# Performance work log

Measured on AMD Instinct MI355X. Metric: run time of the kernel, lower is better.

## Reference

```python
import jax, jax.numpy as jnp
import numpy as np

N = 50000        # nodes
E = 800000       # directed edges
NUM_E = 10000    # hyperedges
NFEAT, NHID, NOUT = 256, 128, 64
K = 10
TEMP = 5.0


def gcn_prop(h, src, dst, n):
    # PyG GCNConv propagation with added self-loops: D^-1/2 (A+I) D^-1/2 h
    ew = jnp.ones(src.shape[0], h.dtype)
    deg = 1.0 + jax.ops.segment_sum(ew, dst, num_segments=n)  # self-loop adds 1
    dinv = jax.lax.rsqrt(deg)
    norm = dinv[src] * dinv[dst]                   # [E]
    out = jax.ops.segment_sum(h[src] * norm[:, None], dst, num_segments=n)
    out = out + h / deg[:, None]                   # self-loop term (weight deg^-1)
    return out


def gcn_conv(x, W, b, src, dst, n):
    return gcn_prop(x @ W, src, dst, n) + b


def hgnnp_conv(x, W, b, hv, he, n, num_e):
    # dhg HGNNPConv: theta(x) then v->e mean aggregation, then e->v mean
    h = x @ W + b
    ones = jnp.ones(hv.shape[0], h.dtype)
    e_deg = jnp.maximum(jax.ops.segment_sum(ones, he, num_segments=num_e), 1.0)
    v_deg = jnp.maximum(jax.ops.segment_sum(ones, hv, num_segments=n), 1.0)
    e_feat = jax.ops.segment_sum(h[hv], he, num_segments=num_e) / e_deg[:, None]
    v_out = jax.ops.segment_sum(e_feat[he], hv, num_segments=n) / v_deg[:, None]
    return v_out


def setup_inputs() -> dict:
    key = jax.random.key(0)
    ks = jax.random.split(key, 12)
    x = jax.random.normal(ks[0], (N, NFEAT), jnp.float32)
    edge_index = jax.random.randint(ks[1], (2, E), 0, N)
    hv_idx = jax.random.randint(ks[2], (200000,), 0, N)
    he_idx = jax.random.randint(ks[3], (200000,), 0, NUM_E)

    def glorot(k, shape):
        lim = float(np.sqrt(6.0 / (shape[0] + shape[1])))
        return jax.random.uniform(k, shape, jnp.float32, -lim, lim)

    return {
        "x": x, "edge_index": edge_index, "hv_idx": hv_idx, "he_idx": he_idx,
        "gcn_W1": glorot(ks[4], (NFEAT, NHID)), "gcn_b1": jnp.zeros((NHID,), jnp.float32),
        "gcn_W2": glorot(ks[5], (NHID, NOUT)), "gcn_b2": jnp.zeros((NOUT,), jnp.float32),
        "hg_W1": glorot(ks[6], (NFEAT, NHID)), "hg_b1": jnp.zeros((NHID,), jnp.float32),
        "hg_W2": glorot(ks[7], (NHID, NOUT)), "hg_b2": jnp.zeros((NOUT,), jnp.float32),
        "num_iter": 1,
    }


def reference(x, edge_index, hv_idx, he_idx,
              gcn_W1, gcn_b1, gcn_W2, gcn_b2,
              hg_W1, hg_b1, hg_W2, hg_b2, num_iter):
    src, dst = edge_index[0], edge_index[1]

    # HGNNP_GCN encoder (dropout is identity in eval-style reference)
    x1 = jax.nn.relu(gcn_conv(x, gcn_W1, gcn_b1, src, dst, N))
    x2 = gcn_conv(x1, gcn_W2, gcn_b2, src, dst, N)
    x3 = jax.nn.relu(hgnnp_conv(x, hg_W1, hg_b1, hv_idx, he_idx, N, NUM_E))
    x4 = hgnnp_conv(x3, hg_W2, hg_b2, hv_idx, he_idx, N, NUM_E)  # is_last: no act
    embeds = x2 * 0.5 + x4 * 0.5                     # [N, NOUT]

    # row-normalize (diag(1/||row||) @ data)
    data = embeds / jnp.linalg.norm(embeds, axis=1, keepdims=True)

    # kmeans++ init is a host-side, data-dependent pick; use deterministic
    # strided row selection from the (detached) normalized embeddings.
    init_idx = jnp.arange(K) * (N // K)
    mu = jax.lax.stop_gradient(data[init_idx])       # [K, NOUT]

    for _ in range(int(num_iter)):
        dist = data @ mu.T                           # [N, K]
        r = jax.nn.softmax(TEMP * dist, axis=1)
        cluster_r = r.sum(axis=0)                    # [K]
        cluster_mean = r.T @ data                    # [K, NOUT]
        mu = cluster_mean / cluster_r[:, None]

    dist = data @ mu.T
    r = jax.nn.softmax(TEMP * dist, axis=1)
    return mu, r, embeds, dist
```

## Files before the change

kernel.cpp:

```cpp
#include <hip/hip_runtime.h>
#include <hip/hip_bf16.h>


#define NN   50000
#define NP   50048
#define EE   800000
#define NINC 200000
#define NEH  10000
#define KCL  10

#define MU_OFF  0
#define R_OFF   640
#define EMB_OFF 500640
#define D_OFF   3700640

typedef __hip_bfloat16 bf16;
typedef unsigned short u16;
typedef unsigned int   u32;
typedef __attribute__((ext_vector_type(8))) short short8;
typedef __attribute__((ext_vector_type(4))) float f32x4;

__device__ __forceinline__ float b2f(bf16 v){ return __bfloat162float(v); }
__device__ __forceinline__ float us2f(u16 u){ return __uint_as_float(((unsigned)u) << 16); }
__device__ __forceinline__ u16 f2bu(float f){
  unsigned u = __float_as_uint(f);
  return (u16)((u + 0x7fffu + ((u >> 16) & 1u)) >> 16);
}
__device__ __forceinline__ bf16 f2b(float f){
  u16 r = f2bu(f);
  bf16 h;
  reinterpret_cast<u16&>(h) = r;
  return h;
}
__device__ __forceinline__ float ldf(const void* p, size_t i, int isbf){
  return isbf ? b2f(((const bf16*)p)[i]) : ((const float*)p)[i];
}
__device__ __forceinline__ void stf(void* p, size_t i, float v, int isbf){
  if (isbf) ((bf16*)p)[i] = f2b(v);
  else      ((float*)p)[i] = v;
}

__global__ void k_detect(const u16* __restrict__ xr, int* flag){
  __shared__ int bad;
  if (threadIdx.x == 0) bad = 0;
  __syncthreads();
  for (int i = threadIdx.x; i < 4096; i += 256){
    int e = (xr[i] >> 7) & 0xFF;
    if (e >= 0xEF) bad = 1;
  }
  __syncthreads();
  if (threadIdx.x == 0) *flag = bad ? 0 : 1;
}

__global__ void k_aconv(const void* __restrict__ x, u16* __restrict__ xb,
                        const int* __restrict__ flag){
  int i = blockIdx.x*256 + threadIdx.x;
  const int n4 = NN*256/4;
  if (i >= n4) return;
  ushort4 o;
  if (flag[0]){
    o = ((const ushort4*)x)[i];
  } else {
    float4 v = ((const float4*)x)[i];
    o = make_ushort4(f2bu(v.x), f2bu(v.y), f2bu(v.z), f2bu(v.w));
  }
  ((ushort4*)xb)[i] = o;
}

__global__ void k_wprep(const void* gW1, const void* hW1, const void* gW2, const void* hW2,
                        const void* gb1, const void* hb1, const void* gb2, const void* hb2,
                        u16* gW1t, u16* hW1t, u16* gW2t, u16* hW2t,
                        float* gb1f, float* hb1f, float* gb2f, float* hb2f,
                        const int* __restrict__ flag){
  const int isbf = flag[0];
  int i = blockIdx.x*256 + threadIdx.x;
  if (i < 256*128){
    int n = i >> 8, k = i & 255;
    gW1t[i] = f2bu(ldf(gW1, (size_t)k*128 + n, isbf));
    hW1t[i] = f2bu(ldf(hW1, (size_t)k*128 + n, isbf));
  }
  if (i < 64*128){
    int n = i >> 7, k = i & 127;
    gW2t[i] = f2bu(ldf(gW2, (size_t)k*64 + n, isbf));
    hW2t[i] = f2bu(ldf(hW2, (size_t)k*64 + n, isbf));
  }
  if (i < 128){ gb1f[i] = ldf(gb1,i,isbf); hb1f[i] = ldf(hb1,i,isbf); }
  if (i < 64) { gb2f[i] = ldf(gb2,i,isbf); hb2f[i] = ldf(hb2,i,isbf); }
}

template<int WORDS, int NRANGE, int NCHUNK>
__global__ __launch_bounds__(256) void k_hist(const int* __restrict__ key,
                                              u32* __restrict__ H, int chunk){
  __shared__ u32 hist[WORDS];
  int r = blockIdx.x / NCHUNK, c = blockIdx.x % NCHUNK;
  for (int i = threadIdx.x; i < WORDS; i += 256) hist[i] = 0;
  __syncthreads();
  int base = c*chunk, lo = r*2*WORDS;
  for (int i = threadIdx.x; i < chunk; i += 256){
    int d = key[base+i] - lo;
    if ((unsigned)d < (unsigned)(2*WORDS))
      atomicAdd(&hist[d < WORDS ? d : d-WORDS], d < WORDS ? 1u : 65536u);
  }
  __syncthreads();
  u32* out = H + (size_t)blockIdx.x*WORDS;
  for (int i = threadIdx.x; i < WORDS; i += 256) out[i] = hist[i];
}

template<int WORDS, int NRANGE, int NCHUNK>
__global__ void k_hscan(u32* __restrict__ H, int* __restrict__ cnt){
  int t = blockIdx.x*256 + threadIdx.x;
  if (t >= NRANGE*WORDS) return;
  int r = t / WORDS, w = t % WORDS;
  u32 run = 0;
  u32* col = H + (size_t)r*NCHUNK*WORDS + w;
  for (int b = 0; b < NCHUNK; ++b){
    u32 v = col[(size_t)b*WORDS];
    col[(size_t)b*WORDS] = run;
    run += v;
  }
  cnt[r*2*WORDS + w]         = (int)(run & 0xffffu);
  cnt[r*2*WORDS + WORDS + w] = (int)(run >> 16);
}

template<int WORDS, int NRANGE, int NCHUNK>
__global__ __launch_bounds__(256) void k_fill2(const int* __restrict__ key,
    const int* __restrict__ val, const u32* __restrict__ H,
    const int* __restrict__ rp, int* __restrict__ csr, int chunk){
  __shared__ u32 cur[WORDS];
  int r = blockIdx.x / NCHUNK, c = blockIdx.x % NCHUNK;
  const u32* pre = H + (size_t)blockIdx.x*WORDS;
  for (int i = threadIdx.x; i < WORDS; i += 256) cur[i] = pre[i];
  __syncthreads();
  int base = c*chunk, lo = r*2*WORDS;
  for (int i = threadIdx.x; i < chunk; i += 256){
    int dd = key[base+i];
    int d = dd - lo;
    if ((unsigned)d < (unsigned)(2*WORDS)){
      bool low = d < WORDS;
      u32 old = atomicAdd(&cur[low ? d : d-WORDS], low ? 1u : 65536u);
      u32 rank = low ? (old & 0xffffu) : (old >> 16);
      csr[rp[dd] + (int)rank] = val[base+i];
    }
  }
}

__global__ void k_invs(const int* __restrict__ cg, const int* __restrict__ cv,
                       const int* __restrict__ ce,
                       float* dinv, float* invv, float* inve){
  int i = blockIdx.x*256 + threadIdx.x;
  if (i < NN){
    float d = 1.0f + (float)cg[i];
    dinv[i] = rsqrtf(d);
    invv[i] = 1.0f / fmaxf((float)cv[i], 1.0f);
  } else if (i < NP){
    dinv[i] = 0.f;
  }
  if (i < NEH) inve[i] = 1.0f / fmaxf((float)ce[i], 1.0f);
}

__global__ void k_scan1_all(const int* cg, const int* cv, const int* ce,
                            int* rp_g, int* rp_v, int* rp_e,
                            int* bs_g, int* bs_v, int* bs_e){
  const int blk = blockIdx.x;
  const int* in; int* out; int* bsum; int n; int lb;
  if (blk < 196){ in=cg; out=rp_g; bsum=bs_g; n=NN; lb=blk; }
  else if (blk < 392){ in=cv; out=rp_v; bsum=bs_v; n=NN; lb=blk-196; }
  else { in=ce; out=rp_e; bsum=bs_e; n=NEH; lb=blk-392; }
  __shared__ int s[256];
  int t = threadIdx.x, i = lb*256 + t;
  int v = (i < n) ? in[i] : 0;
  s[t] = v; __syncthreads();
  #pragma unroll
  for (int off = 1; off < 256; off <<= 1){
    int add = (t >= off) ? s[t-off] : 0;
    __syncthreads();
    s[t] += add;
    __syncthreads();
  }
  if (i < n) out[i] = s[t] - v;
  if (t == 255) bsum[lb] = s[255];
}

__global__ void k_scan2_all(int* bs_g, int* bs_v, int* bs_e){
  int* bsum; int nb;
  if (blockIdx.x == 0){ bsum = bs_g; nb = 196; }
  else if (blockIdx.x == 1){ bsum = bs_v; nb = 196; }
  else { bsum = bs_e; nb = 40; }
  __shared__ int s[256];
  int t = threadIdx.x;
  int v = (t < nb) ? bsum[t] : 0;
  s[t] = v; __syncthreads();
  #pragma unroll
  for (int off = 1; off < 256; off <<= 1){
    int add = (t >= off) ? s[t-off] : 0;
    __syncthreads();
    s[t] += add;
    __syncthreads();
  }
  if (t < nb) bsum[t] = s[t] - v;
}

__global__ void k_scan3_all(int* rp_g, int* rp_v, int* rp_e,
                            const int* bs_g, const int* bs_v, const int* bs_e){
  const int blk = blockIdx.x;
  int* rp; const int* bsum; int n; int lb;
  if (blk < 196){ rp=rp_g; bsum=bs_g; n=NN; lb=blk; }
  else if (blk < 392){ rp=rp_v; bsum=bs_v; n=NN; lb=blk-196; }
  else { rp=rp_e; bsum=bs_e; n=NEH; lb=blk-392; }
  int i = lb*256 + threadIdx.x;
  if (i < n) rp[i] += bsum[lb];
}

template<int KDIM, int NCOL>
__global__ __launch_bounds__(256) void k_gemm_mfma(
    const u16* __restrict__ A, const u16* __restrict__ Wt,
    const float* __restrict__ bias, const float* __restrict__ rowscale,
    u16* __restrict__ C, int relu)
{
  constexpr int NT  = NCOL/16;
  constexpr int LDA = 40;
  __shared__ __align__(16) u16 Asl[64][LDA];
  __shared__ __align__(16) u16 Wsl[NCOL][LDA];
  const int tid  = threadIdx.x;
  const int wave = tid >> 6, lane = tid & 63;
  const int l15 = lane & 15, l4 = lane >> 4;
  const int row0 = blockIdx.x * 64;
  const int ar = tid >> 2, aq = tid & 3;
  constexpr int NW = NCOL*4/256;

  f32x4 acc[NT] = {};

  for (int kk = 0; kk < KDIM; kk += 32){
    {
      uint4 v = *(const uint4*)(A + (size_t)(row0 + ar)*KDIM + kk + aq*8);
      *(uint4*)&Asl[ar][aq*8] = v;
    }
    #pragma unroll
    for (int w2 = 0; w2 < NW; ++w2){
      int c = tid + w2*256;
      int n = c >> 2, q = c & 3;
      uint4 v = *(const uint4*)(Wt + (size_t)n*KDIM + kk + q*8);
      *(uint4*)&Wsl[n][q*8] = v;
    }
    __syncthreads();
    short8 af = *(const short8*)&Asl[wave*16 + l15][l4*8];
    #pragma unroll
    for (int t = 0; t < NT; ++t){
      short8 bf = *(const short8*)&Wsl[t*16 + l15][l4*8];
      acc[t] = __builtin_amdgcn_mfma_f32_16x16x32_bf16(af, bf, acc[t], 0, 0, 0);
    }
    __syncthreads();
  }

  #pragma unroll
  for (int t = 0; t < NT; ++t){
    int gcol = t*16 + l15;
    float b = bias ? bias[gcol] : 0.f;
    #pragma unroll
    for (int e = 0; e < 4; ++e){
      int grow = row0 + wave*16 + l4*4 + e;
      float v = acc[t][e] + b;
      if (relu) v = fmaxf(v, 0.f);
      if (rowscale) v *= rowscale[grow];
      C[(size_t)grow*NCOL + gcol] = f2bu(v);
    }
  }
}

template<int F, bool OUTBF, bool SELF>
__global__ __launch_bounds__(256) void k_gather(
    const int* __restrict__ rp, const int* __restrict__ cnt,
    const int* __restrict__ csr, const float* __restrict__ scale,
    const u16* __restrict__ h, const float* __restrict__ bias,
    void* __restrict__ out, int relu)
{
  const int wave = threadIdx.x >> 6, lane = threadIdx.x & 63;
  const int d = blockIdx.x*4 + wave;
  const int k0 = rp[d], n = cnt[d];

  if constexpr (F == 128){
    const uint* h32 = (const uint*)h;
    float a0=0,a1=0,b0=0,b1=0,c0=0,c1=0,e0=0,e1=0;
    if (SELF){
      uint v = h32[(size_t)d*64 + lane];
      a0 = us2f((u16)v); a1 = us2f((u16)(v>>16));
    }
    for (int base = 0; base < n; base += 64){
      int mm = n - base; if (mm > 64) mm = 64;
      int idx = (lane < mm) ? csr[k0 + base + lane] : 0;
      int jj = 0;
      for (; jj + 4 <= mm; jj += 4){
        int s0=__shfl(idx,jj), s1=__shfl(idx,jj+1), s2=__shfl(idx,jj+2), s3=__shfl(idx,jj+3);
        uint v0 = h32[(size_t)s0*64 + lane];
        uint v1 = h32[(size_t)s1*64 + lane];
        uint v2 = h32[(size_t)s2*64 + lane];
        uint v3 = h32[(size_t)s3*64 + lane];
        a0 += us2f((u16)v0); a1 += us2f((u16)(v0>>16));
        b0 += us2f((u16)v1); b1 += us2f((u16)(v1>>16));
        c0 += us2f((u16)v2); c1 += us2f((u16)(v2>>16));
        e0 += us2f((u16)v3); e1 += us2f((u16)(v3>>16));
      }
      for (; jj < mm; ++jj){
        int s = __shfl(idx, jj);
        uint v = h32[(size_t)s*64 + lane];
        a0 += us2f((u16)v); a1 += us2f((u16)(v>>16));
      }
    }
    float sc = scale[d];
    float o0 = ((a0+b0)+(c0+e0))*sc;
    float o1 = ((a1+b1)+(c1+e1))*sc;
    if (bias){ o0 += bias[lane*2]; o1 += bias[lane*2+1]; }
    if (relu){ o0 = fmaxf(o0,0.f); o1 = fmaxf(o1,0.f); }
    if (OUTBF){
      ((uint*)out)[(size_t)d*64 + lane] = (uint)f2bu(o0) | ((uint)f2bu(o1) << 16);
    } else {
      ((float2*)out)[(size_t)d*64 + lane] = make_float2(o0, o1);
    }
  } else {
    float a=0,b=0,c=0,e=0;
    if (SELF) a = us2f(h[(size_t)d*64 + lane]);
    for (int base = 0; base < n; base += 64){
      int mm = n - base; if (mm > 64) mm = 64;
      int idx = (lane < mm) ? csr[k0 + base + lane] : 0;
      int jj = 0;
      for (; jj + 4 <= mm; jj += 4){
        int s0=__shfl(idx,jj), s1=__shfl(idx,jj+1), s2=__shfl(idx,jj+2), s3=__shfl(idx,jj+3);
        a += us2f(h[(size_t)s0*64 + lane]);
        b += us2f(h[(size_t)s1*64 + lane]);
        c += us2f(h[(size_t)s2*64 + lane]);
        e += us2f(h[(size_t)s3*64 + lane]);
      }
      for (; jj < mm; ++jj){
        int s = __shfl(idx, jj);
        a += us2f(h[(size_t)s*64 + lane]);
      }
    }
    float o = ((a+b)+(c+e))*scale[d];
    if (bias) o += bias[lane];
    if (relu) o = fmaxf(o, 0.f);
    if (OUTBF) ((u16*)out)[(size_t)d*64 + lane] = f2bu(o);
    else       ((float*)out)[(size_t)d*64 + lane] = o;
  }
}

__global__ void k_embeds(const float* __restrict__ x2, const float* __restrict__ x4,
                         void* __restrict__ out, float* __restrict__ data,
                         const int* __restrict__ flag){
  int row  = blockIdx.x*4 + (threadIdx.x >> 6);
  int lane = threadIdx.x & 63;
  if (row >= NN) return;
  size_t idx = (size_t)row*64 + lane;
  float v = 0.5f*(x2[idx] + x4[idx]);
  float ss = v*v;
  #pragma unroll
  for (int off=32; off>0; off>>=1) ss += __shfl_xor(ss, off);
  float inv = rsqrtf(ss);
  data[idx] = v*inv;
  stf(out, EMB_OFF + idx, v, flag[0]);
}

__global__ void k_mu_init(const float* __restrict__ data, float* __restrict__ mu){
  int p = blockIdx.x*256 + threadIdx.x;
  if (p >= KCL*64) return;
  int k = p >> 6, f = p & 63;
  mu[p] = data[(size_t)k*(NN/KCL)*64 + f];
}

__global__ __launch_bounds__(128) void k_cluster_accum(const float* __restrict__ data,
    const float* __restrict__ mu, float* csum, float* cr, const int* nit, int iter)
{
  if (iter >= nit[0]) return;
  __shared__ float dt[128][65];
  __shared__ float rl[128][KCL];
  __shared__ float ms[KCL*64];
  int tid = threadIdx.x;
  int rowbase = blockIdx.x*128;
  for (int j=tid; j<KCL*64; j+=128) ms[j] = mu[j];
  for (int j=tid; j<128*64; j+=128){
    int rr = j>>6, f = j&63;
    int row = rowbase + rr;
    dt[rr][f] = (row<NN) ? data[(size_t)row*64+f] : 0.f;
  }
  __syncthreads();
  {
    int row = rowbase + tid;
    float dot[KCL];
    #pragma unroll
    for (int k2=0;k2<KCL;k2++) dot[k2]=0.f;
    for (int f=0; f<64; f++){
      float a = dt[tid][f];
      #pragma unroll
      for (int k2=0;k2<KCL;k2++) dot[k2] = fmaf(a, ms[k2*64+f], dot[k2]);
    }
    float m = -1e30f;
    #pragma unroll
    for (int k2=0;k2<KCL;k2++) m = fmaxf(m, 5.0f*dot[k2]);
    float s = 0.f, ev[KCL];
    #pragma unroll
    for (int k2=0;k2<KCL;k2++){ ev[k2] = expf(5.0f*dot[k2]-m); s += ev[k2]; }
    float inv = 1.0f/s;
    #pragma unroll
    for (int k2=0;k2<KCL;k2++) rl[tid][k2] = (row<NN) ? ev[k2]*inv : 0.f;
  }
  __syncthreads();
  for (int p=tid; p<KCL*64; p+=128){
    int k2 = p>>6, f = p&63;
    float acc = 0.f;
    for (int r2=0;r2<128;r2++) acc += rl[r2][k2]*dt[r2][f];
    unsafeAtomicAdd(&csum[p], acc);
  }
  if (tid < KCL){
    float acc = 0.f;
    for (int r2=0;r2<128;r2++) acc += rl[r2][tid];
    unsafeAtomicAdd(&cr[tid], acc);
  }
}

__global__ void k_mu_update(float* mu, float* csum, float* cr, const int* nit, int iter){
  if (iter >= nit[0]) return;
  int p = threadIdx.x;
  float c = csum[p];
  float r = cr[p>>6];
  __syncthreads();
  mu[p] = c / r;
  csum[p] = 0.f;
  if (p < KCL) cr[p] = 0.f;
}

__global__ __launch_bounds__(128) void k_cluster_final(const float* __restrict__ data,
    const float* __restrict__ mu, void* __restrict__ out, const int* __restrict__ flag)
{
  __shared__ float dt[128][65];
  __shared__ float ms[KCL*64];
  int tid = threadIdx.x;
  int rowbase = blockIdx.x*128;
  for (int j=tid; j<KCL*64; j+=128) ms[j] = mu[j];
  for (int j=tid; j<128*64; j+=128){
    int rr = j>>6, f = j&63;
    int row = rowbase + rr;
    dt[rr][f] = (row<NN) ? data[(size_t)row*64+f] : 0.f;
  }
  __syncthreads();
  int row = rowbase + tid;
  if (row >= NN) return;
  int isbf = flag[0];
  float dot[KCL];
  #pragma unroll
  for (int k2=0;k2<KCL;k2++) dot[k2]=0.f;
  for (int f=0; f<64; f++){
    float a = dt[tid][f];
    #pragma unroll
    for (int k2=0;k2<KCL;k2++) dot[k2] = fmaf(a, ms[k2*64+f], dot[k2]);
  }
  float m = -1e30f;
  #pragma unroll
  for (int k2=0;k2<KCL;k2++) m = fmaxf(m, 5.0f*dot[k2]);
  float s = 0.f, ev[KCL];
  #pragma unroll
  for (int k2=0;k2<KCL;k2++){ ev[k2] = expf(5.0f*dot[k2]-m); s += ev[k2]; }
  float inv = 1.0f/s;
  #pragma unroll
  for (int k2=0;k2<KCL;k2++){
    stf(out, (size_t)D_OFF + (size_t)row*KCL + k2, dot[k2],     isbf);
    stf(out, (size_t)R_OFF + (size_t)row*KCL + k2, ev[k2]*inv,  isbf);
  }
}

__global__ void k_mu_out(const float* __restrict__ mu, void* __restrict__ out,
                         const int* __restrict__ flag){
  int p = blockIdx.x*256 + threadIdx.x;
  if (p < KCL*64) stf(out, MU_OFF + p, mu[p], flag[0]);
}

extern "C" void kernel_launch(void* const* d_in, const int* in_sizes, int n_in,
                              void* d_out, int out_size, void* d_ws, size_t ws_size,
                              hipStream_t stream)
{
  const void* x   = d_in[0];
  const int*  ei  = (const int*)d_in[1];
  const int*  hv  = (const int*)d_in[2];
  const int*  he  = (const int*)d_in[3];
  const void* gW1 = d_in[4];
  const void* gb1 = d_in[5];
  const void* gW2 = d_in[6];
  const void* gb2 = d_in[7];
  const void* hW1 = d_in[8];
  const void* hb1 = d_in[9];
  const void* hW2 = d_in[10];
  const void* hb2 = d_in[11];
  const int*  nit = (const int*)d_in[12];

  float* ws = (float*)d_ws;
  size_t o = 0;
  u16*   xb  = (u16*)(ws + o); o += (size_t)NP*128;
  u16*   BAb = (u16*)(ws + o); o += (size_t)NP*64;
  u16*   BBb = (u16*)(ws + o); o += (size_t)NP*64;
  u16*   BCb = (u16*)(ws + o); o += (size_t)NP*64;
  u16*   BDb = (u16*)(ws + o); o += (size_t)NEH*64;
  u16*  gW1t = (u16*)(ws + o); o += 16384;
  u16*  hW1t = (u16*)(ws + o); o += 16384;
  u16*  gW2t = (u16*)(ws + o); o += 4096;
  u16*  hW2t = (u16*)(ws + o); o += 4096;
  float* gb1f = ws + o; o += 128;
  float* hb1f = ws + o; o += 128;
  float* gb2f = ws + o; o += 64;
  float* hb2f = ws + o; o += 64;
  float* dinv = ws + o; o += 50048;
  float* invv = ws + o; o += 50048;
  float* inve = ws + o; o += 10048;
  float* mu   = ws + o; o += 640;
  float* csum = ws + o; o += 640;
  float* cr   = ws + o; o += 64;
  int*   dflg = (int*)(ws + o); o += 16;
  float* x2f   = (float*)xb;
  float* x4f   = (float*)xb + (size_t)NP*64;
  float* dataf = (float*)BBb;
  int* ib = (int*)(ws + o);
  size_t io = 0;
  int* cg    = ib + io; io += NN;
  int* cv    = ib + io; io += NN;
  int* ce    = ib + io; io += NEH + 48;
  int* rp_g  = ib + io; io += NN;
  int* rp_v  = ib + io; io += NN;
  int* rp_e  = ib + io; io += NEH + 48;
  int* csr_g = ib + io; io += EE;
  int* csr_e = ib + io; io += NINC;
  int* csr_v = ib + io; io += NINC;
  int* bs_g  = ib + io; io += 256;
  int* bs_v  = ib + io; io += 256;
  int* bs_e  = ib + io; io += 256;
  u32* Hg = (u32*)(ib + io); io += 2*64*12500;
  u32* Hv = (u32*)(ib + io); io += 2*64*12500;
  u32* He = (u32*)(ib + io); io += 64*5000;

  const int* srcp = ei;
  const int* dstp = ei + EE;
  dim3 B(256);
  const int NBP = (NP + 255)/256;

  k_detect<<<dim3(1), B, 0, stream>>>((const u16*)x, dflg);
  k_aconv<<<dim3(12500), B, 0, stream>>>(x, xb, dflg);
  k_wprep<<<dim3(128), B, 0, stream>>>(gW1, hW1, gW2, hW2, gb1, hb1, gb2, hb2,
                                       gW1t, hW1t, gW2t, hW2t,
                                       gb1f, hb1f, gb2f, hb2f, dflg);

  k_hist<12500,2,64><<<dim3(128), B, 0, stream>>>(dstp, Hg, 12500);
  k_hist<12500,2,64><<<dim3(128), B, 0, stream>>>(hv,   Hv, 3125);
  k_hist< 5000,1,64><<<dim3( 64), B, 0, stream>>>(he,   He, 3125);
  k_hscan<12500,2,64><<<dim3(98), B, 0, stream>>>(Hg, cg);
  k_hscan<12500,2,64><<<dim3(98), B, 0, stream>>>(Hv, cv);
  k_hscan< 5000,1,64><<<dim3(20), B, 0, stream>>>(He, ce);
  k_invs<<<dim3(NBP), B, 0, stream>>>(cg, cv, ce, dinv, invv, inve);
  k_scan1_all<<<dim3(432), B, 0, stream>>>(cg, cv, ce, rp_g, rp_v, rp_e, bs_g, bs_v, bs_e);
  k_scan2_all<<<dim3(3),   B, 0, stream>>>(bs_g, bs_v, bs_e);
  k_scan3_all<<<dim3(432), B, 0, stream>>>(rp_g, rp_v, rp_e, bs_g, bs_v, bs_e);
  k_fill2<12500,2,64><<<dim3(128), B, 0, stream>>>(dstp, srcp, Hg, rp_g, csr_g, 12500);
  k_fill2<12500,2,64><<<dim3(128), B, 0, stream>>>(hv,   he,   Hv, rp_v, csr_v, 3125);
  k_fill2< 5000,1,64><<<dim3( 64), B, 0, stream>>>(he,   hv,   He, rp_e, csr_e, 3125);

  const int NB = NP/64;
  k_gemm_mfma<256,128><<<dim3(NB), B, 0, stream>>>(xb, gW1t, nullptr, dinv, BAb, 0);
  k_gather<128,true,true><<<dim3(NN/4), B, 0, stream>>>(rp_g, cg, csr_g, dinv,
                                                        BAb, gb1f, BBb, 1);
  k_gemm_mfma<256,128><<<dim3(NB), B, 0, stream>>>(xb, hW1t, hb1f, nullptr, BAb, 0);
  k_gather<128,true,false><<<dim3(NEH/4), B, 0, stream>>>(rp_e, ce, csr_e, inve,
                                                          BAb, nullptr, BDb, 0);
  k_gather<128,true,false><<<dim3(NN/4), B, 0, stream>>>(rp_v, cv, csr_v, invv,
                                                         BDb, nullptr, BCb, 1);
  k_gemm_mfma<128,64><<<dim3(NB), B, 0, stream>>>(BBb, gW2t, nullptr, dinv, BAb, 0);
  k_gather<64,false,true><<<dim3(NN/4), B, 0, stream>>>(rp_g, cg, csr_g, dinv,
                                                        BAb, gb2f, x2f, 0);
  k_gemm_mfma<128,64><<<dim3(NB), B, 0, stream>>>(BCb, hW2t, hb2f, nullptr, BAb, 0);
  k_gather<64,true,false><<<dim3(NEH/4), B, 0, stream>>>(rp_e, ce, csr_e, inve,
                                                         BAb, nullptr, BDb, 0);
  k_gather<64,false,false><<<dim3(NN/4), B, 0, stream>>>(rp_v, cv, csr_v, invv,
                                                         BDb, nullptr, x4f, 0);

  k_embeds<<<dim3((NN+3)/4), B, 0, stream>>>(x2f, x4f, d_out, dataf, dflg);

  k_mu_init<<<dim3(3), B, 0, stream>>>(dataf, mu);
  hipMemsetAsync(csum, 0, (640+64)*4, stream);
  const int CB = (NN + 127)/128;
  for (int it = 0; it < 4; ++it){
    k_cluster_accum<<<dim3(CB), dim3(128), 0, stream>>>(dataf, mu, csum, cr, nit, it);
    k_mu_update    <<<dim3(1),  dim3(640), 0, stream>>>(mu, csum, cr, nit, it);
  }
  k_cluster_final<<<dim3(CB), dim3(128), 0, stream>>>(dataf, mu, d_out, dflg);
  k_mu_out       <<<dim3(3),  B, 0, stream>>>(mu, d_out, dflg);
}
```

Baseline: 390.0 us.

## Replace packed 16-bit histogram counters with plain per-bin counters over more ranges

The CSR build's chunked histogram used two 16-bit counters packed per 32-bit shared word to cover 25000 keys per block. It now uses one 32-bit counter per bin over 6250-key ranges and launches 4x as many blocks. The fill kernel adds the row pointer into the shared cursor up front, so each element does one atomicAdd and a direct write with no unpacking or rp[dd] global load. In exchange each block rescans its whole input chunk with more ranges, so total key reads rise, and the scan kernels touch more histogram memory.

New measurement: 391.7 us. Within noise of the previous version (+0.4%).

```diff
diff --git a/kernel.cpp b/kernel.cpp
--- a/kernel.cpp
+++ b/kernel.cpp
@@ -88,58 +88,55 @@
   if (i < 64) { gb2f[i] = ldf(gb2,i,isbf); hb2f[i] = ldf(hb2,i,isbf); }
 }
 
-template<int WORDS, int NRANGE, int NCHUNK>
-__global__ __launch_bounds__(256) void k_hist(const int* __restrict__ key,
-                                              u32* __restrict__ H, int chunk){
-  __shared__ u32 hist[WORDS];
+template<int BINS, int NCHUNK>
+__global__ __launch_bounds__(256) void k_hist2(const int* __restrict__ key,
+                                               u32* __restrict__ H, int chunk){
+  __shared__ u32 hist[BINS];
   int r = blockIdx.x / NCHUNK, c = blockIdx.x % NCHUNK;
-  for (int i = threadIdx.x; i < WORDS; i += 256) hist[i] = 0;
-  __syncthreads();
-  int base = c*chunk, lo = r*2*WORDS;
+  for (int i = threadIdx.x; i < BINS; i += 256) hist[i] = 0;
+  __syncthreads();
+  int base = c*chunk, lo = r*BINS;
   for (int i = threadIdx.x; i < chunk; i += 256){
     int d = key[base+i] - lo;
-    if ((unsigned)d < (unsigned)(2*WORDS))
-      atomicAdd(&hist[d < WORDS ? d : d-WORDS], d < WORDS ? 1u : 65536u);
-  }
-  __syncthreads();
-  u32* out = H + (size_t)blockIdx.x*WORDS;
-  for (int i = threadIdx.x; i < WORDS; i += 256) out[i] = hist[i];
-}
-
-template<int WORDS, int NRANGE, int NCHUNK>
-__global__ void k_hscan(u32* __restrict__ H, int* __restrict__ cnt){
+    if ((unsigned)d < (unsigned)BINS) atomicAdd(&hist[d], 1u);
+  }
+  __syncthreads();
+  u32* out = H + (size_t)blockIdx.x*BINS;
+  for (int i = threadIdx.x; i < BINS; i += 256) out[i] = hist[i];
+}
+
+template<int BINS, int NCHUNK, int NRANGE>
+__global__ void k_hscan2(u32* __restrict__ H, int* __restrict__ cnt){
   int t = blockIdx.x*256 + threadIdx.x;
-  if (t >= NRANGE*WORDS) return;
-  int r = t / WORDS, w = t % WORDS;
+  if (t >= NRANGE*BINS) return;
+  int r = t / BINS, w = t % BINS;
   u32 run = 0;
-  u32* col = H + (size_t)r*NCHUNK*WORDS + w;
+  u32* col = H + (size_t)r*NCHUNK*BINS + w;
   for (int b = 0; b < NCHUNK; ++b){
-    u32 v = col[(size_t)b*WORDS];
-    col[(size_t)b*WORDS] = run;
+    u32 v = col[(size_t)b*BINS];
+    col[(size_t)b*BINS] = run;
     run += v;
   }
-  cnt[r*2*WORDS + w]         = (int)(run & 0xffffu);
-  cnt[r*2*WORDS + WORDS + w] = (int)(run >> 16);
-}
-
-template<int WORDS, int NRANGE, int NCHUNK>
-__global__ __launch_bounds__(256) void k_fill2(const int* __restrict__ key,
+  cnt[t] = (int)run;
+}
+
+template<int BINS, int NCHUNK>
+__global__ __launch_bounds__(256) void k_fill3(const int* __restrict__ key,
     const int* __restrict__ val, const u32* __restrict__ H,
     const int* __restrict__ rp, int* __restrict__ csr, int chunk){
-  __shared__ u32 cur[WORDS];
+  __shared__ u32 cur[BINS];
   int r = blockIdx.x / NCHUNK, c = blockIdx.x % NCHUNK;
-  const u32* pre = H + (size_t)blockIdx.x*WORDS;
-  for (int i = threadIdx.x; i < WORDS; i += 256) cur[i] = pre[i];
-  __syncthreads();
-  int base = c*chunk, lo = r*2*WORDS;
+  const u32* pre = H + (size_t)blockIdx.x*BINS;
+  const int* rps = rp + r*BINS;
+  for (int i = threadIdx.x; i < BINS; i += 256) cur[i] = pre[i] + (u32)rps[i];
+  __syncthreads();
+  int base = c*chunk, lo = r*BINS;
   for (int i = threadIdx.x; i < chunk; i += 256){
     int dd = key[base+i];
     int d = dd - lo;
-    if ((unsigned)d < (unsigned)(2*WORDS)){
-      bool low = d < WORDS;
-      u32 old = atomicAdd(&cur[low ? d : d-WORDS], low ? 1u : 65536u);
-      u32 rank = low ? (old & 0xffffu) : (old >> 16);
-      csr[rp[dd] + (int)rank] = val[base+i];
+    if ((unsigned)d < (unsigned)BINS){
+      u32 pos = atomicAdd(&cur[d], 1u);
+      csr[pos] = val[base+i];
     }
   }
 }
@@ -529,9 +526,9 @@
   int* bs_g  = ib + io; io += 256;
   int* bs_v  = ib + io; io += 256;
   int* bs_e  = ib + io; io += 256;
-  u32* Hg = (u32*)(ib + io); io += 2*64*12500;
-  u32* Hv = (u32*)(ib + io); io += 2*64*12500;
-  u32* He = (u32*)(ib + io); io += 64*5000;
+  u32* Hg = (u32*)(ib + io); io += 512*6250;
+  u32* Hv = (u32*)(ib + io); io += 512*6250;
+  u32* He = (u32*)(ib + io); io += 128*5000;
 
   const int* srcp = ei;
   const int* dstp = ei + EE;
@@ -544,19 +541,19 @@
                                        gW1t, hW1t, gW2t, hW2t,
                                        gb1f, hb1f, gb2f, hb2f, dflg);
 
-  k_hist<12500,2,64><<<dim3(128), B, 0, stream>>>(dstp, Hg, 12500);
-  k_hist<12500,2,64><<<dim3(128), B, 0, stream>>>(hv,   Hv, 3125);
-  k_hist< 5000,1,64><<<dim3( 64), B, 0, stream>>>(he,   He, 3125);
-  k_hscan<12500,2,64><<<dim3(98), B, 0, stream>>>(Hg, cg);
-  k_hscan<12500,2,64><<<dim3(98), B, 0, stream>>>(Hv, cv);
-  k_hscan< 5000,1,64><<<dim3(20), B, 0, stream>>>(He, ce);
+  k_hist2<6250,64><<<dim3(512), B, 0, stream>>>(dstp, Hg, 12500);
+  k_hist2<6250,64><<<dim3(512), B, 0, stream>>>(hv,   Hv, 3125);
+  k_hist2<5000,64><<<dim3(128), B, 0, stream>>>(he,   He, 3125);
+  k_hscan2<6250,64,8><<<dim3(196), B, 0, stream>>>(Hg, cg);
+  k_hscan2<6250,64,8><<<dim3(196), B, 0, stream>>>(Hv, cv);
+  k_hscan2<5000,64,2><<<dim3(40),  B, 0, stream>>>(He, ce);
   k_invs<<<dim3(NBP), B, 0, stream>>>(cg, cv, ce, dinv, invv, inve);
   k_scan1_all<<<dim3(432), B, 0, stream>>>(cg, cv, ce, rp_g, rp_v, rp_e, bs_g, bs_v, bs_e);
   k_scan2_all<<<dim3(3),   B, 0, stream>>>(bs_g, bs_v, bs_e);
   k_scan3_all<<<dim3(432), B, 0, stream>>>(rp_g, rp_v, rp_e, bs_g, bs_v, bs_e);
-  k_fill2<12500,2,64><<<dim3(128), B, 0, stream>>>(dstp, srcp, Hg, rp_g, csr_g, 12500);
-  k_fill2<12500,2,64><<<dim3(128), B, 0, stream>>>(hv,   he,   Hv, rp_v, csr_v, 3125);
-  k_fill2< 5000,1,64><<<dim3( 64), B, 0, stream>>>(he,   hv,   He, rp_e, csr_e, 3125);
+  k_fill3<6250,64><<<dim3(512), B, 0, stream>>>(dstp, srcp, Hg, rp_g, csr_g, 12500);
+  k_fill3<6250,64><<<dim3(512), B, 0, stream>>>(hv,   he,   Hv, rp_v, csr_v, 3125);
+  k_fill3<5000,64><<<dim3(128), B, 0, stream>>>(he,   hv,   He, rp_e, csr_e, 3125);
 
   const int NB = NP/64;
   k_gemm_mfma<256,128><<<dim3(NB), B, 0, stream>>>(xb, gW1t, nullptr, dinv, BAb, 0);
```
